# Optimization experiments

Hardware: AMD Instinct MI355X
Metric: run time of the kernel (lower is better)

The kernel has to match this reference:

```python
import jax, jax.numpy as jnp
import numpy as np

N = 4096      # num nodes
E = 131072    # num edges
D = 128       # embed dim (in=out)
HID = 16      # kan hidden dim
G, K = 4, 3   # KAN grid_size / spline_order (GCN + FFN kans)
GA, KA = 2, 1 # attention KANLinear grid_size / spline_order
H, HD = 8, 16 # heads, head_dim

def make_grid(in_f, g, k):
    h = 2.0 / g
    pts = (np.arange(-k, g + k + 1) * h - 1.0).astype(np.float32)  # [g+2k+1]
    return jnp.asarray(np.tile(pts[None, :], (in_f, 1)))            # [in_f, g+2k+1]

GRID_D = make_grid(D, G, K)
GRID_H = make_grid(HID, G, K)
GRID_A = make_grid(D, GA, KA)

def b_splines(x, grid, k):
    # x: [n, in] -> B-spline bases [n, in, g+k] via Cox-de-Boor recursion
    x = x[:, :, None]
    g = grid[None]
    bases = ((x >= g[..., :-1]) & (x < g[..., 1:])).astype(x.dtype)
    for j in range(1, k + 1):
        bases = ((x - g[..., :-(j + 1)]) / (g[..., j:-1] - g[..., :-(j + 1)]) * bases[..., :-1]
                 + (g[..., j + 1:] - x) / (g[..., j + 1:] - g[..., 1:-j]) * bases[..., 1:])
    return bases

def kan_lin(x, bw, sw, grid, k, use_silu):
    base = jax.nn.silu(x) if use_silu else x
    return base @ bw.T + jnp.einsum('nig,oig->no', b_splines(x, grid, k), sw)

def ekan2(x, bw1, sw1, bw2, sw2):
    # eKAN with layers_hidden=[D, HID, D], SiLU base activation
    h = kan_lin(x, bw1, sw1, GRID_D, K, True)
    return kan_lin(h, bw2, sw2, GRID_H, K, True)

def layer_norm(h, s, b):
    m = jnp.mean(h, axis=-1, keepdims=True)
    v = jnp.var(h, axis=-1, keepdims=True)
    return (h - m) * jax.lax.rsqrt(v + 1e-5) * s + b

def setup_inputs() -> dict:
    key = jax.random.key(0)
    ks = jax.random.split(key, 20)
    r = lambda i, shape: jax.random.normal(ks[i], shape, jnp.float32) * 0.1
    return dict(
        x=jax.random.normal(ks[0], (N, D), jnp.float32),
        edge_index=jax.random.randint(ks[1], (2, E), 0, N),
        gcn_bw1=r(2, (HID, D)), gcn_sw1=r(3, (HID, D, G + K)),
        gcn_bw2=r(4, (D, HID)), gcn_sw2=r(5, (D, HID, G + K)),
        q_bw=r(6, (D, D)), q_sw=r(7, (D, D, GA + KA)),
        k_bw=r(8, (D, D)), k_sw=r(9, (D, D, GA + KA)),
        v_bw=r(10, (D, D)), v_sw=r(11, (D, D, GA + KA)),
        ffn_bw1=r(12, (HID, D)), ffn_sw1=r(13, (HID, D, G + K)),
        ffn_bw2=r(14, (D, HID)), ffn_sw2=r(15, (D, HID, G + K)),
        ln1_s=jnp.ones(D), ln1_b=jnp.zeros(D),
        ln2_s=jnp.ones(D), ln2_b=jnp.zeros(D),
        ln3_s=jnp.ones(D), ln3_b=jnp.zeros(D),
    )

def reference(x, edge_index, gcn_bw1, gcn_sw1, gcn_bw2, gcn_sw2,
              q_bw, q_sw, k_bw, k_sw, v_bw, v_sw,
              ffn_bw1, ffn_sw1, ffn_bw2, ffn_sw2,
              ln1_s, ln1_b, ln2_s, ln2_b, ln3_s, ln3_b):
    n = x.shape[0]
    # ---- local GCN-KAN branch: KAN(A_hat x) ----
    loops = jnp.arange(n)
    row = jnp.concatenate([edge_index[0], loops])  # sources (+ self-loops)
    col = jnp.concatenate([edge_index[1], loops])  # targets
    w = jnp.ones(row.shape[0], x.dtype)
    deg = jax.ops.segment_sum(w, row, num_segments=n)
    dis = jnp.where(deg > 0, deg ** -0.5, 0.0)
    norm = dis[row] * w * dis[col]
    agg = jax.ops.segment_sum(norm[:, None] * x[row], col, num_segments=n)  # [n, D]
    h_local = ekan2(agg, gcn_bw1, gcn_sw1, gcn_bw2, gcn_sw2)
    h_local = layer_norm(x + h_local, ln1_s, ln1_b)
    # ---- global KAN multi-head attention branch ----
    Q = kan_lin(x, q_bw, q_sw, GRID_A, KA, False).reshape(n, H, HD)
    Kv = kan_lin(x, k_bw, k_sw, GRID_A, KA, False).reshape(n, H, HD)
    V = kan_lin(x, v_bw, v_sw, GRID_A, KA, False).reshape(n, H, HD)
    scores = jnp.einsum('nhd,mhd->hnm', Q, Kv) / np.sqrt(HD)  # [H, n, n]
    attn = jax.nn.softmax(scores, axis=-1)
    h_attn = jnp.einsum('hnm,mhd->nhd', attn, V).reshape(n, D)
    h_attn = layer_norm(x + h_attn, ln2_s, ln2_b)
    # ---- combine + KAN feed-forward ----
    h = h_local + h_attn
    out = layer_norm(h + ekan2(h, ffn_bw1, ffn_sw1, ffn_bw2, ffn_sw2), ln3_s, ln3_b)
    return out
```

## Files before the change

### kernel.cpp

```cpp
#include <hip/hip_runtime.h>

typedef unsigned short u16;
typedef unsigned int u32;

#define D_ 128
#define HID_ 16
#define NH_ 8
#define HD_ 16
#define PSTRIDE 17

#define WE_W1G 0
#define WE_W2G 16384
#define WE_W1F 32768
#define WE_W2F 49152
#define WE_TOTAL 65536

#define KROW 24
#define VROW 136
#define PROW 40
#define HROW 136

typedef __attribute__((ext_vector_type(8))) short bfrag;
typedef __attribute__((ext_vector_type(4))) float ffrag;


__device__ __forceinline__ float bf2f(u16 u) {
    union { u32 i; float f; } v; v.i = ((u32)u) << 16; return v.f;
}
__device__ __forceinline__ u16 f2bf(float f) {
    u32 x = __float_as_uint(f);
    u32 r = (x + 0x7fffu + ((x >> 16) & 1u)) >> 16;
    return (u16)r;
}
__device__ __forceinline__ float rdf(const void* p, int i, bool bf) {
    return bf ? bf2f(((const u16*)p)[i]) : ((const float*)p)[i];
}

__device__ __forceinline__ u32 probe_stat(const u16* p) {
    for (int i = 0; i < 128; i++) {
        u16 u = p[i];
        int e = (u >> 7) & 0xFF;
        int m = u & 0x7F;
        bool zero = (e == 0) && (m == 0);
        bool sane = zero || (e >= 97 && e <= 147);
        if (!sane) return 0u;
    }
    return 1u;
}

__global__ void k_detect(const void* x,
                         const void* gbw1, const void* gsw1, const void* gbw2, const void* gsw2,
                         const void* qbw, const void* qsw, const void* kbw, const void* ksw,
                         const void* vbw, const void* vsw,
                         const void* fbw1, const void* fsw1, const void* fbw2, const void* fsw2,
                         const void* l1s, const void* l1b, const void* l2s, const void* l2b,
                         const void* l3s, const void* l3b,
                         u32* flags) {
    int t = threadIdx.x;
    const void* ptrs[21] = {x, gbw1, gsw1, gbw2, gsw2, qbw, qsw, kbw, ksw, vbw, vsw,
                            fbw1, fsw1, fbw2, fsw2, l1s, l1b, l2s, l2b, l3s, l3b};
    if (t < 21) {
        u32 f = 0;
        if (t == 15 || t == 17 || t == 19) {
            f = (((const u32*)ptrs[t])[0] != 0x3F800000u) ? 1u : 0u;
        } else if (t == 16 || t == 18 || t == 20) {
            f = 0;
        } else {
            f = probe_stat((const u16*)ptrs[t]);
        }
        flags[t] = f;
    }
    __syncthreads();
    if (t == 16 || t == 18 || t == 20) flags[t] = flags[t - 1];
}

__device__ __forceinline__ float cub_seg(float s) {
    if (s < 0.0f || s >= 4.0f) return 0.0f;
    if (s < 1.0f) return s * s * s * (1.0f / 6.0f);
    if (s < 2.0f) { float r = s - 1.0f; return (1.0f + 3.0f * r + 3.0f * r * r - 3.0f * r * r * r) * (1.0f / 6.0f); }
    if (s < 3.0f) { float r = s - 2.0f; return (4.0f - 6.0f * r * r + 3.0f * r * r * r) * (1.0f / 6.0f); }
    float q = 4.0f - s; return q * q * q * (1.0f / 6.0f);
}
__device__ __forceinline__ float lin_seg(float s) {
    if (s < 0.0f || s >= 2.0f) return 0.0f;
    return (s < 1.0f) ? s : (2.0f - s);
}

__device__ __forceinline__ float bsum(float v, float* tmp) {
#pragma unroll
    for (int off = 1; off < 64; off <<= 1) v += __shfl_xor(v, off, 64);
    __syncthreads();
    if ((threadIdx.x & 63) == 0) tmp[threadIdx.x >> 6] = v;
    __syncthreads();
    return tmp[0] + tmp[1];
}

__device__ __forceinline__ uint4 feat8(float a) {
    float si = a / (1.0f + __expf(-a));
    float u = (a + 2.5f) * 2.0f;
    float b0 = cub_seg(u), b1 = cub_seg(u - 1.0f), b2 = cub_seg(u - 2.0f), b3 = cub_seg(u - 3.0f);
    float b4 = cub_seg(u - 4.0f), b5 = cub_seg(u - 5.0f), b6 = cub_seg(u - 6.0f);
    uint4 r;
    r.x = (u32)f2bf(si) | ((u32)f2bf(b0) << 16);
    r.y = (u32)f2bf(b1) | ((u32)f2bf(b2) << 16);
    r.z = (u32)f2bf(b3) | ((u32)f2bf(b4) << 16);
    r.w = (u32)f2bf(b5) | ((u32)f2bf(b6) << 16);
    return r;
}

__global__ void k_conv4(const void* __restrict__ x,
                        const void* l1s, const void* l1b, const void* l2s,
                        const void* l2b, const void* l3s, const void* l3b,
                        const u32* __restrict__ flags,
                        float* __restrict__ xin, float* __restrict__ lnp,
                        u16* __restrict__ F,
                        int* __restrict__ cnt, int* __restrict__ fill,
                        int* __restrict__ degi, int N) {
    int total = N * D_ + 768 + 3 * N;
    bool bfx = flags[0] != 0;
    for (int i = blockIdx.x * 256 + threadIdx.x; i < total; i += gridDim.x * 256) {
        if (i < N * D_) {
            float xv = rdf(x, i, bfx);
            xin[i] = xv;
            float u = xv + 2.0f;
            u32 lo = (u32)f2bf(xv) | ((u32)f2bf(lin_seg(u)) << 16);
            u32 hi = (u32)f2bf(lin_seg(u - 1.0f)) | ((u32)f2bf(lin_seg(u - 2.0f)) << 16);
            ((uint2*)F)[i] = make_uint2(lo, hi);
        } else {
            int j = i - N * D_;
            if (j < 768) {
                int sel = j >> 7, k = j & 127;
                const void* p = sel == 0 ? l1s : sel == 1 ? l1b : sel == 2 ? l2s
                             : sel == 3 ? l2b : sel == 4 ? l3s : l3b;
                lnp[j] = rdf(p, k, flags[15 + sel] != 0);
            } else {
                int j2 = j - 768;
                if (j2 < N) cnt[j2] = 0;
                else if (j2 < 2 * N) fill[j2 - N] = 0;
                else degi[j2 - 2 * N] = 0;
            }
        }
    }
}

__global__ void k_pack(const void* gbw1, const void* gsw1, const void* gbw2, const void* gsw2,
                       const void* fbw1, const void* fsw1, const void* fbw2, const void* fsw2,
                       const void* qbw, const void* qsw, const void* kbw, const void* ksw,
                       const void* vbw, const void* vsw,
                       const u32* __restrict__ flags,
                       u16* __restrict__ Web, u16* __restrict__ Wb) {
    int t = blockIdx.x * 256 + threadIdx.x;
    if (t < 8192) {
        int seg = t >> 11, i = t & 2047;
        const void* bw = seg == 0 ? gbw1 : seg == 1 ? gbw2 : seg == 2 ? fbw1 : fbw2;
        const void* sw = seg == 0 ? gsw1 : seg == 1 ? gsw2 : seg == 2 ? fsw1 : fsw2;
        int fb = seg == 0 ? 1 : seg == 1 ? 3 : seg == 2 ? 11 : 13;
        bool bwbf = flags[fb] != 0, swbf = flags[fb + 1] != 0;
        u16* dst = Web + (size_t)seg * 16384 + (size_t)i * 8;
        dst[0] = f2bf(rdf(bw, i, bwbf));
#pragma unroll
        for (int g = 0; g < 7; g++) dst[1 + g] = f2bf(rdf(sw, i * 7 + g, swbf));
    } else if (t < 8192 + 49152) {
        int uu = t - 8192;
        int seg = uu >> 14, i = uu & 16383;
        const void* bw = seg == 0 ? qbw : seg == 1 ? kbw : vbw;
        const void* sw = seg == 0 ? qsw : seg == 1 ? ksw : vsw;
        int fb = 5 + seg * 2;
        bool bwbf = flags[fb] != 0, swbf = flags[fb + 1] != 0;
        float sc = (seg == 0) ? 0.25f : 1.0f;
        u16* dst = Wb + (size_t)seg * 65536 + (size_t)i * 4;
        dst[0] = f2bf(rdf(bw, i, bwbf) * sc);
#pragma unroll
        for (int g = 0; g < 3; g++) dst[1 + g] = f2bf(rdf(sw, i * 3 + g, swbf) * sc);
    }
}

__global__ void k_count(const int* __restrict__ ei, int* __restrict__ cnt,
                        int* __restrict__ degi, int E) {
    int e = blockIdx.x * 256 + threadIdx.x;
    if (e < E) {
        atomicAdd(&degi[ei[e]], 1);
        atomicAdd(&cnt[ei[E + e]], 1);
    }
}
__global__ __launch_bounds__(1024) void k_scan(const int* __restrict__ cnt,
                                               const int* __restrict__ degi,
                                               int* __restrict__ rowptr,
                                               float* __restrict__ dis, int N) {
    __shared__ int s[1024];
    int t = threadIdx.x;
    int base = t * 4;
    int a[4];
#pragma unroll
    for (int k = 0; k < 4; k++) a[k] = (base + k < N) ? cnt[base + k] : 0;
    int loc = a[0] + a[1] + a[2] + a[3];
    s[t] = loc;
    __syncthreads();
    for (int off = 1; off < 1024; off <<= 1) {
        int v = (t >= off) ? s[t - off] : 0;
        __syncthreads();
        s[t] += v;
        __syncthreads();
    }
    int ex = s[t] - loc;
    int run = ex;
#pragma unroll
    for (int k = 0; k < 4; k++) {
        if (base + k < N) rowptr[base + k] = run;
        run += a[k];
    }
    if (t == 1023) rowptr[N] = s[1023];
#pragma unroll
    for (int k = 0; k < 4; k++)
        if (base + k < N) dis[base + k] = rsqrtf((float)degi[base + k] + 1.0f);
}
__global__ void k_fill(const int* __restrict__ ei, const int* __restrict__ rowptr,
                       int* __restrict__ fill, int* __restrict__ elist, int E) {
    int e = blockIdx.x * 256 + threadIdx.x;
    if (e < E) {
        int r = ei[e], c = ei[E + e];
        int pos = rowptr[c] + atomicAdd(&fill[c], 1);
        elist[pos] = r;
    }
}

__global__ __launch_bounds__(128) void k_gcn(const int* __restrict__ rowptr,
        const int* __restrict__ elist, const float* __restrict__ dis,
        const float* __restrict__ xin, u16* __restrict__ Afeat) {
    int c = blockIdx.x, t = threadIdx.x;
    __shared__ int ids[128];
    __shared__ float wsh[128];
    int beg = rowptr[c], end = rowptr[c + 1];
    float acc = 0.0f;
    for (int j0 = beg; j0 < end; j0 += 128) {
        int cc = min(128, end - j0);
        __syncthreads();
        if (t < cc) {
            int rr = elist[j0 + t];
            ids[t] = rr;
            wsh[t] = dis[rr];
        }
        __syncthreads();
        for (int j = 0; j < cc; j++)
            acc += wsh[j] * xin[(size_t)ids[j] * D_ + t];
    }
    float dc = dis[c];
    float a = dc * (acc + dc * xin[(size_t)c * D_ + t]);
    ((uint4*)Afeat)[(size_t)c * D_ + t] = feat8(a);
}

__global__ __launch_bounds__(64) void k_ekan_mm(const u16* __restrict__ A,
        const u16* __restrict__ W1b, const u16* __restrict__ W2b,
        const float* __restrict__ resid,
        const float* __restrict__ lns, const float* __restrict__ lnb,
        void* __restrict__ outp, const u32* __restrict__ flags, int fin, int N) {
    __shared__ u16 hfL[16 * HROW];
    int mt = blockIdx.x;
    int lane = threadIdx.x, quad = lane >> 4, l15 = lane & 15;
    const u16* ar = A + (size_t)(mt * 16 + l15) * 1024 + quad * 8;
    const u16* br = W1b + (size_t)l15 * 1024 + quad * 8;
    ffrag acc = {0, 0, 0, 0};
#pragma unroll
    for (int ks = 0; ks < 1024; ks += 32) {
        bfrag af = *(const bfrag*)(ar + ks);
        bfrag bf = *(const bfrag*)(br + ks);
        acc = __builtin_amdgcn_mfma_f32_16x16x32_bf16(af, bf, acc, 0, 0, 0);
    }
#define G1EPI(RR, COMP) { \
    uint4 fv = feat8(acc.COMP); \
    *(uint4*)(&hfL[(quad * 4 + RR) * HROW + l15 * 8]) = fv; }
    G1EPI(0, x) G1EPI(1, y) G1EPI(2, z) G1EPI(3, w)
#undef G1EPI
    __asm__ volatile("s_waitcnt lgkmcnt(0)" ::: "memory");
    __builtin_amdgcn_wave_barrier();
    const u16* b0 = W2b + (size_t)l15 * 128 + quad * 8;
    ffrag a0 = {0,0,0,0}, a1 = {0,0,0,0}, a2 = {0,0,0,0}, a3 = {0,0,0,0};
    ffrag a4 = {0,0,0,0}, a5 = {0,0,0,0}, a6 = {0,0,0,0}, a7 = {0,0,0,0};
#pragma unroll
    for (int ks = 0; ks < 128; ks += 32) {
        bfrag af = *(const bfrag*)(&hfL[l15 * HROW + quad * 8 + ks]);
        a0 = __builtin_amdgcn_mfma_f32_16x16x32_bf16(af, *(const bfrag*)(b0 + 0 * 2048 + ks), a0, 0, 0, 0);
        a1 = __builtin_amdgcn_mfma_f32_16x16x32_bf16(af, *(const bfrag*)(b0 + 1 * 2048 + ks), a1, 0, 0, 0);
        a2 = __builtin_amdgcn_mfma_f32_16x16x32_bf16(af, *(const bfrag*)(b0 + 2 * 2048 + ks), a2, 0, 0, 0);
        a3 = __builtin_amdgcn_mfma_f32_16x16x32_bf16(af, *(const bfrag*)(b0 + 3 * 2048 + ks), a3, 0, 0, 0);
        a4 = __builtin_amdgcn_mfma_f32_16x16x32_bf16(af, *(const bfrag*)(b0 + 4 * 2048 + ks), a4, 0, 0, 0);
        a5 = __builtin_amdgcn_mfma_f32_16x16x32_bf16(af, *(const bfrag*)(b0 + 5 * 2048 + ks), a5, 0, 0, 0);
        a6 = __builtin_amdgcn_mfma_f32_16x16x32_bf16(af, *(const bfrag*)(b0 + 6 * 2048 + ks), a6, 0, 0, 0);
        a7 = __builtin_amdgcn_mfma_f32_16x16x32_bf16(af, *(const bfrag*)(b0 + 7 * 2048 + ks), a7, 0, 0, 0);
    }
    float ls0 = lns[l15],       lb0 = lnb[l15];
    float ls1 = lns[16 + l15],  lb1 = lnb[16 + l15];
    float ls2 = lns[32 + l15],  lb2 = lnb[32 + l15];
    float ls3 = lns[48 + l15],  lb3 = lnb[48 + l15];
    float ls4 = lns[64 + l15],  lb4 = lnb[64 + l15];
    float ls5 = lns[80 + l15],  lb5 = lnb[80 + l15];
    float ls6 = lns[96 + l15],  lb6 = lnb[96 + l15];
    float ls7 = lns[112 + l15], lb7 = lnb[112 + l15];
    bool bfo = (fin != 0) && (flags[0] != 0);
#define G2EPI(RR, COMP) { \
    int node = mt * 16 + quad * 4 + RR; \
    const float* rr_ = resid + (size_t)node * 128 + l15; \
    float v0 = a0.COMP + rr_[0];   float v1 = a1.COMP + rr_[16]; \
    float v2 = a2.COMP + rr_[32];  float v3 = a3.COMP + rr_[48]; \
    float v4 = a4.COMP + rr_[64];  float v5 = a5.COMP + rr_[80]; \
    float v6 = a6.COMP + rr_[96];  float v7 = a7.COMP + rr_[112]; \
    float s1 = ((v0 + v1) + (v2 + v3)) + ((v4 + v5) + (v6 + v7)); \
    float s2 = ((v0*v0 + v1*v1) + (v2*v2 + v3*v3)) + ((v4*v4 + v5*v5) + (v6*v6 + v7*v7)); \
    s1 += __shfl_xor(s1, 1, 64); s2 += __shfl_xor(s2, 1, 64); \
    s1 += __shfl_xor(s1, 2, 64); s2 += __shfl_xor(s2, 2, 64); \
    s1 += __shfl_xor(s1, 4, 64); s2 += __shfl_xor(s2, 4, 64); \
    s1 += __shfl_xor(s1, 8, 64); s2 += __shfl_xor(s2, 8, 64); \
    float mean = s1 * 0.0078125f; \
    float var = s2 * 0.0078125f - mean * mean; \
    float rs = rsqrtf(var + 1e-5f); \
    float y0 = (v0 - mean) * rs * ls0 + lb0; float y1 = (v1 - mean) * rs * ls1 + lb1; \
    float y2 = (v2 - mean) * rs * ls2 + lb2; float y3 = (v3 - mean) * rs * ls3 + lb3; \
    float y4 = (v4 - mean) * rs * ls4 + lb4; float y5 = (v5 - mean) * rs * ls5 + lb5; \
    float y6 = (v6 - mean) * rs * ls6 + lb6; float y7 = (v7 - mean) * rs * ls7 + lb7; \
    if (bfo) { \
        u16* ob = (u16*)outp + (size_t)node * 128 + l15; \
        ob[0] = f2bf(y0); ob[16] = f2bf(y1); ob[32] = f2bf(y2); ob[48] = f2bf(y3); \
        ob[64] = f2bf(y4); ob[80] = f2bf(y5); ob[96] = f2bf(y6); ob[112] = f2bf(y7); \
    } else { \
        float* ob = (float*)outp + (size_t)node * 128 + l15; \
        ob[0] = y0; ob[16] = y1; ob[32] = y2; ob[48] = y3; \
        ob[64] = y4; ob[80] = y5; ob[96] = y6; ob[112] = y7; \
    } }
    G2EPI(0, x) G2EPI(1, y) G2EPI(2, z) G2EPI(3, w)
#undef G2EPI
}

#define QKV_STORE(ACC, TL) { \
    int col = cg * 48 + (TL) * 16 + l15; \
    int mat = col >> 7, idx = col & 127; \
    u16* dstb = (mat == 0) ? Qb : (mat == 1) ? Kb : Vb; \
    size_t base = (size_t)(idx >> 4) * N * HD_ + (size_t)(idx & 15); \
    dstb[base + (size_t)(rowb + 0) * HD_] = f2bf(ACC.x); \
    dstb[base + (size_t)(rowb + 1) * HD_] = f2bf(ACC.y); \
    dstb[base + (size_t)(rowb + 2) * HD_] = f2bf(ACC.z); \
    dstb[base + (size_t)(rowb + 3) * HD_] = f2bf(ACC.w); \
}

__global__ __launch_bounds__(64) void k_qkv5(const u16* __restrict__ F,
        const u16* __restrict__ Wb,
        u16* __restrict__ Qb, u16* __restrict__ Kb, u16* __restrict__ Vb, int N) {
    int mt = blockIdx.x, cg = blockIdx.y;
    int lane = threadIdx.x, quad = lane >> 4, l15 = lane & 15;
    const u16* arow = F + (size_t)(mt * 16 + l15) * 512 + quad * 8;
    const u16* b0r = Wb + (size_t)(cg * 48 + l15) * 512 + quad * 8;
    const u16* b1r = b0r + 16 * 512;
    const u16* b2r = b0r + 32 * 512;
    ffrag a0 = {0, 0, 0, 0}, a1 = {0, 0, 0, 0}, a2 = {0, 0, 0, 0};
#pragma unroll
    for (int ks = 0; ks < 512; ks += 32) {
        bfrag af = *(const bfrag*)(arow + ks);
        bfrag bf0 = *(const bfrag*)(b0r + ks);
        bfrag bf1 = *(const bfrag*)(b1r + ks);
        bfrag bf2 = *(const bfrag*)(b2r + ks);
        a0 = __builtin_amdgcn_mfma_f32_16x16x32_bf16(af, bf0, a0, 0, 0, 0);
        a1 = __builtin_amdgcn_mfma_f32_16x16x32_bf16(af, bf1, a1, 0, 0, 0);
        a2 = __builtin_amdgcn_mfma_f32_16x16x32_bf16(af, bf2, a2, 0, 0, 0);
    }
    int rowb = mt * 16 + quad * 4;
    QKV_STORE(a0, 0)
    QKV_STORE(a1, 1)
    QKV_STORE(a2, 2)
}

#define ATTN_SCORE(QF, LACC, PBT) { \
    ffrag zz = {0.0f, 0.0f, 0.0f, 0.0f}; \
    ffrag s0 = __builtin_amdgcn_mfma_f32_16x16x32_bf16(QF, kf0, zz, 0, 0, 0); \
    ffrag s1 = __builtin_amdgcn_mfma_f32_16x16x32_bf16(QF, kf1, zz, 0, 0, 0); \
    float a0 = __expf(s0.x), a1 = __expf(s0.y), a2 = __expf(s0.z), a3 = __expf(s0.w); \
    float b0 = __expf(s1.x), b1 = __expf(s1.y), b2 = __expf(s1.z), b3 = __expf(s1.w); \
    LACC.x += a0 + b0; LACC.y += a1 + b1; LACC.z += a2 + b2; LACC.w += a3 + b3; \
    u32* pw = (u32*)PBT; \
    pw[(quad * 4 + 0) * (PROW / 2) + l15] = (__float_as_uint(a0) >> 16) | (__float_as_uint(b0) & 0xFFFF0000u); \
    pw[(quad * 4 + 1) * (PROW / 2) + l15] = (__float_as_uint(a1) >> 16) | (__float_as_uint(b1) & 0xFFFF0000u); \
    pw[(quad * 4 + 2) * (PROW / 2) + l15] = (__float_as_uint(a2) >> 16) | (__float_as_uint(b2) & 0xFFFF0000u); \
    pw[(quad * 4 + 3) * (PROW / 2) + l15] = (__float_as_uint(a3) >> 16) | (__float_as_uint(b3) & 0xFFFF0000u); \
}

#define ATTN_PV(OACC, PBT) { \
    bfrag pf = *(const bfrag*)(&PBT[l15 * PROW + quad * 8]); \
    OACC = __builtin_amdgcn_mfma_f32_16x16x32_bf16(pf, vf, OACC, 0, 0, 0); \
}

#define STORE_TILE(OACC, LACC, TL) { \
    int q0 = qtb + (TL) * 16 + quad * 4; \
    float* pp; \
    pp = part + ((size_t)(h * N + q0 + 0) * SPLIT + s) * PSTRIDE; \
    pp[1 + l15] = OACC.x; if (l15 == 0) pp[0] = LACC.x; \
    pp = part + ((size_t)(h * N + q0 + 1) * SPLIT + s) * PSTRIDE; \
    pp[1 + l15] = OACC.y; if (l15 == 0) pp[0] = LACC.y; \
    pp = part + ((size_t)(h * N + q0 + 2) * SPLIT + s) * PSTRIDE; \
    pp[1 + l15] = OACC.z; if (l15 == 0) pp[0] = LACC.z; \
    pp = part + ((size_t)(h * N + q0 + 3) * SPLIT + s) * PSTRIDE; \
    pp[1 + l15] = OACC.w; if (l15 == 0) pp[0] = LACC.w; \
}

__global__ __launch_bounds__(256) void k_attn9(const u16* __restrict__ Qb,
        const u16* __restrict__ Kb, const u16* __restrict__ Vb,
        float* __restrict__ part, int N, int SPLIT) {
    int s = blockIdx.x, qb = blockIdx.y, h = blockIdx.z;
    int t = threadIdx.x;
    int w = t >> 6, lane = t & 63, quad = lane >> 4, l15 = lane & 15;
    __shared__ u16 ldsK[128 * KROW + 16];
    __shared__ u16 ldsVt[16 * VROW];
    __shared__ u16 ldsP[4][4][16 * PROW];

    const u16* qrow = Qb + (size_t)h * N * HD_;
    const u16* krow = Kb + (size_t)h * N * HD_;
    const u16* vrow = Vb + (size_t)h * N * HD_;

    for (int i = t; i < (128 * KROW + 16) / 2; i += 256) ((u32*)ldsK)[i] = 0;

    int qtb = qb * 256 + w * 64;
    bfrag qz = {0, 0, 0, 0, 0, 0, 0, 0};
    bfrag qf0 = qz, qf1 = qz, qf2 = qz, qf3 = qz;
    if (quad < 2) {
        qf0 = *(const bfrag*)(qrow + (size_t)(qtb + 0 * 16 + l15) * HD_ + quad * 8);
        qf1 = *(const bfrag*)(qrow + (size_t)(qtb + 1 * 16 + l15) * HD_ + quad * 8);
        qf2 = *(const bfrag*)(qrow + (size_t)(qtb + 2 * 16 + l15) * HD_ + quad * 8);
        qf3 = *(const bfrag*)(qrow + (size_t)(qtb + 3 * 16 + l15) * HD_ + quad * 8);
    }

    ffrag o0 = {0, 0, 0, 0}, o1 = {0, 0, 0, 0}, o2 = {0, 0, 0, 0}, o3 = {0, 0, 0, 0};
    ffrag L0 = {0, 0, 0, 0}, L1 = {0, 0, 0, 0}, L2 = {0, 0, 0, 0}, L3 = {0, 0, 0, 0};
    u16* pb0 = &ldsP[w][0][0];
    u16* pb1 = &ldsP[w][1][0];
    u16* pb2 = &ldsP[w][2][0];
    u16* pb3 = &ldsP[w][3][0];

    int keys = N / SPLIT;
    int kstart0 = s * keys;
    for (int kst = 0; kst < keys; kst += 128) {
        int kg = kstart0 + kst;
        __syncthreads();
        if (t < 128) {
            const uint4* src = (const uint4*)(krow + (size_t)(kg + t) * HD_);
            uint4 a = src[0], b = src[1];
            *(uint4*)(&ldsK[t * KROW]) = a;
            *(uint4*)(&ldsK[t * KROW + 8]) = b;
        } else {
            int key = t - 128;
            const uint4* src = (const uint4*)(vrow + (size_t)(kg + key) * HD_);
            uint4 a = src[0], b = src[1];
            ldsVt[0 * VROW + key] = (u16)(a.x);  ldsVt[1 * VROW + key] = (u16)(a.x >> 16);
            ldsVt[2 * VROW + key] = (u16)(a.y);  ldsVt[3 * VROW + key] = (u16)(a.y >> 16);
            ldsVt[4 * VROW + key] = (u16)(a.z);  ldsVt[5 * VROW + key] = (u16)(a.z >> 16);
            ldsVt[6 * VROW + key] = (u16)(a.w);  ldsVt[7 * VROW + key] = (u16)(a.w >> 16);
            ldsVt[8 * VROW + key] = (u16)(b.x);  ldsVt[9 * VROW + key] = (u16)(b.x >> 16);
            ldsVt[10 * VROW + key] = (u16)(b.y); ldsVt[11 * VROW + key] = (u16)(b.y >> 16);
            ldsVt[12 * VROW + key] = (u16)(b.z); ldsVt[13 * VROW + key] = (u16)(b.z >> 16);
            ldsVt[14 * VROW + key] = (u16)(b.w); ldsVt[15 * VROW + key] = (u16)(b.w >> 16);
        }
        __syncthreads();
#pragma unroll
        for (int koff = 0; koff < 128; koff += 32) {
            bfrag kf0 = *(const bfrag*)(&ldsK[(koff + 2 * l15) * KROW + quad * 8]);
            bfrag kf1 = *(const bfrag*)(&ldsK[(koff + 2 * l15 + 1) * KROW + quad * 8]);
            bfrag vf = *(const bfrag*)(&ldsVt[l15 * VROW + koff + quad * 8]);
            ATTN_SCORE(qf0, L0, pb0)
            ATTN_SCORE(qf1, L1, pb1)
            ATTN_SCORE(qf2, L2, pb2)
            ATTN_SCORE(qf3, L3, pb3)
            __asm__ volatile("s_waitcnt lgkmcnt(0)" ::: "memory");
            ATTN_PV(o0, pb0)
            ATTN_PV(o1, pb1)
            ATTN_PV(o2, pb2)
            ATTN_PV(o3, pb3)
        }
    }

#pragma unroll
    for (int off = 1; off < 16; off <<= 1) {
        L0.x += __shfl_xor(L0.x, off, 64); L0.y += __shfl_xor(L0.y, off, 64);
        L0.z += __shfl_xor(L0.z, off, 64); L0.w += __shfl_xor(L0.w, off, 64);
        L1.x += __shfl_xor(L1.x, off, 64); L1.y += __shfl_xor(L1.y, off, 64);
        L1.z += __shfl_xor(L1.z, off, 64); L1.w += __shfl_xor(L1.w, off, 64);
        L2.x += __shfl_xor(L2.x, off, 64); L2.y += __shfl_xor(L2.y, off, 64);
        L2.z += __shfl_xor(L2.z, off, 64); L2.w += __shfl_xor(L2.w, off, 64);
        L3.x += __shfl_xor(L3.x, off, 64); L3.y += __shfl_xor(L3.y, off, 64);
        L3.z += __shfl_xor(L3.z, off, 64); L3.w += __shfl_xor(L3.w, off, 64);
    }
    STORE_TILE(o0, L0, 0)
    STORE_TILE(o1, L1, 1)
    STORE_TILE(o2, L2, 2)
    STORE_TILE(o3, L3, 3)
}

__global__ __launch_bounds__(128) void k_comb(const float* __restrict__ part,
        const float* __restrict__ xin, const float* __restrict__ hl,
        const float* __restrict__ lnp, float* __restrict__ hv,
        u16* __restrict__ Afeat, int N, int SPLIT) {
    int n = blockIdx.x, t = threadIdx.x;
    __shared__ float red[128];
    int h = t >> 4, d = t & 15;
    float L = 0.0f, O = 0.0f;
    for (int ss = 0; ss < SPLIT; ss++) {
        const float* ps = part + ((size_t)(h * N + n) * SPLIT + ss) * PSTRIDE;
        L += ps[0];
        O += ps[1 + d];
    }
    float ha = O / L;
    float r = xin[(size_t)n * D_ + t] + ha;
    float mean = bsum(r, red) * (1.0f / 128.0f);
    float c = r - mean;
    float var = bsum(c * c, red) * (1.0f / 128.0f);
    float y2 = c * rsqrtf(var + 1e-5f) * lnp[256 + t] + lnp[384 + t];
    float hvv = hl[(size_t)n * D_ + t] + y2;
    hv[(size_t)n * D_ + t] = hvv;
    ((uint4*)Afeat)[(size_t)n * D_ + t] = feat8(hvv);
}

extern "C" void kernel_launch(void* const* d_in, const int* in_sizes, int n_in,
                              void* d_out, int out_size, void* d_ws, size_t ws_size,
                              hipStream_t stream) {
    const void* x = d_in[0];
    const int* ei = (const int*)d_in[1];
    const void* gbw1 = d_in[2];
    const void* gsw1 = d_in[3];
    const void* gbw2 = d_in[4];
    const void* gsw2 = d_in[5];
    const void* qbw = d_in[6];
    const void* qsw = d_in[7];
    const void* kbw = d_in[8];
    const void* ksw = d_in[9];
    const void* vbw = d_in[10];
    const void* vsw = d_in[11];
    const void* fbw1 = d_in[12];
    const void* fsw1 = d_in[13];
    const void* fbw2 = d_in[14];
    const void* fsw2 = d_in[15];
    const void* ln1s = d_in[16];
    const void* ln1b = d_in[17];
    const void* ln2s = d_in[18];
    const void* ln2b = d_in[19];
    const void* ln3s = d_in[20];
    const void* ln3b = d_in[21];

    const int N = in_sizes[0] / D_;
    const int E = in_sizes[1] / 2;
    const size_t ND = (size_t)N * D_;

    float* wf = (float*)d_ws;
    u32* flags = (u32*)wf;
    float* lnp = wf + 32;
    float* dis = wf + 800;
    float* xin = dis + N;
    float* hl  = xin + ND;
    float* hv  = hl + ND;
    u16* Web = (u16*)(hv + ND);
    u16* Wb  = Web + WE_TOTAL;
    u16* F   = Wb + 196608;
    u16* Qb  = F + (size_t)N * 512;
    u16* Kb  = Qb + ND;
    u16* Vb  = Kb + ND;
    u16* Afeat = Vb + ND;
    int* cnt    = (int*)(Afeat + (size_t)N * 1024);
    int* fill   = cnt + N;
    int* degi   = fill + N;
    int* rowptr = degi + N;
    int* elist  = rowptr + N + 1;
    float* part = (float*)(elist + E);

    size_t baseBytes = (size_t)((char*)part - (char*)d_ws);
    int SPLIT = 16;
    if (baseBytes + (size_t)NH_ * N * 16 * PSTRIDE * 4 > ws_size) SPLIT = 8;
    if (baseBytes + (size_t)NH_ * N * 8 * PSTRIDE * 4 > ws_size) SPLIT = 4;

    k_detect<<<1, 64, 0, stream>>>(x, gbw1, gsw1, gbw2, gsw2, qbw, qsw, kbw, ksw,
                                   vbw, vsw, fbw1, fsw1, fbw2, fsw2,
                                   ln1s, ln1b, ln2s, ln2b, ln3s, ln3b, flags);
    k_conv4<<<1024, 256, 0, stream>>>(x, ln1s, ln1b, ln2s, ln2b, ln3s, ln3b,
                                      flags, xin, lnp, F, cnt, fill, degi, N);
    k_pack<<<224, 256, 0, stream>>>(gbw1, gsw1, gbw2, gsw2, fbw1, fsw1, fbw2, fsw2,
                                    qbw, qsw, kbw, ksw, vbw, vsw, flags, Web, Wb);
    k_count<<<(E + 255) / 256, 256, 0, stream>>>(ei, cnt, degi, E);
    k_scan<<<1, 1024, 0, stream>>>(cnt, degi, rowptr, dis, N);
    k_fill<<<(E + 255) / 256, 256, 0, stream>>>(ei, rowptr, fill, elist, E);
    k_gcn<<<N, 128, 0, stream>>>(rowptr, elist, dis, xin, Afeat);
    k_ekan_mm<<<N / 16, 64, 0, stream>>>(Afeat, Web + WE_W1G, Web + WE_W2G, xin,
                                         lnp + 0, lnp + 128, hl, flags, 0, N);
    k_qkv5<<<dim3(N / 16, 8), 64, 0, stream>>>(F, Wb, Qb, Kb, Vb, N);
    k_attn9<<<dim3(SPLIT, N / 256, NH_), 256, 0, stream>>>(Qb, Kb, Vb, part, N, SPLIT);
    k_comb<<<N, 128, 0, stream>>>(part, xin, hl, lnp, hv, Afeat, N, SPLIT);
    k_ekan_mm<<<N / 16, 64, 0, stream>>>(Afeat, Web + WE_W1F, Web + WE_W2F, hv,
                                         lnp + 512, lnp + 640, d_out, flags, 1, N);
}
```

Before: 244.2 us.

## Merge setup kernels, warp-shuffle scan, exp2 softmax, halve attention split

Folds the conversion, weight packing and edge counting kernels into one launch and moves the counter zeroing into the detect kernel, cutting launch count and serialization. It also rewrites the single-block prefix scan to use wavefront shuffles instead of a barrier-heavy shared-memory loop. The GCN gather loop gets two accumulators, and attention uses exp2 with log2(e) folded into the Q scale. The default attention split drops from 16 to 8, which changes parallelism against partial-combine work. Zeroing 3N ints from a single 256-thread block adds serial work at the start.

```diff
diff --git a/kernel.cpp b/kernel.cpp
--- a/kernel.cpp
+++ b/kernel.cpp
@@ -20,8 +20,19 @@
 #define PROW 40
 #define HROW 136
 
+#define QSCALE 0.3606737602222409f
+
 typedef __attribute__((ext_vector_type(8))) short bfrag;
 typedef __attribute__((ext_vector_type(4))) float ffrag;
+
+#if defined(__has_builtin)
+#if __has_builtin(__builtin_amdgcn_exp2f)
+#define EXP2F(x) __builtin_amdgcn_exp2f(x)
+#endif
+#endif
+#ifndef EXP2F
+#define EXP2F(x) exp2f(x)
+#endif
 
 
 __device__ __forceinline__ float bf2f(u16 u) {
@@ -48,14 +59,14 @@
     return 1u;
 }
 
-__global__ void k_detect(const void* x,
+__global__ __launch_bounds__(256) void k_detect(const void* x,
                          const void* gbw1, const void* gsw1, const void* gbw2, const void* gsw2,
                          const void* qbw, const void* qsw, const void* kbw, const void* ksw,
                          const void* vbw, const void* vsw,
                          const void* fbw1, const void* fsw1, const void* fbw2, const void* fsw2,
                          const void* l1s, const void* l1b, const void* l2s, const void* l2b,
                          const void* l3s, const void* l3b,
-                         u32* flags) {
+                         u32* flags, int* __restrict__ cnt3, int N) {
     int t = threadIdx.x;
     const void* ptrs[21] = {x, gbw1, gsw1, gbw2, gsw2, qbw, qsw, kbw, ksw, vbw, vsw,
                             fbw1, fsw1, fbw2, fsw2, l1s, l1b, l2s, l2b, l3s, l3b};
@@ -72,6 +83,8 @@
     }
     __syncthreads();
     if (t == 16 || t == 18 || t == 20) flags[t] = flags[t - 1];
+    int tot = 3 * N;
+    for (int i = t; i < tot; i += 256) cnt3[i] = 0;
 }
 
 __device__ __forceinline__ float cub_seg(float s) {
@@ -108,112 +121,114 @@
     return r;
 }
 
-__global__ void k_conv4(const void* __restrict__ x,
-                        const void* l1s, const void* l1b, const void* l2s,
-                        const void* l2b, const void* l3s, const void* l3b,
-                        const u32* __restrict__ flags,
-                        float* __restrict__ xin, float* __restrict__ lnp,
-                        u16* __restrict__ F,
-                        int* __restrict__ cnt, int* __restrict__ fill,
-                        int* __restrict__ degi, int N) {
-    int total = N * D_ + 768 + 3 * N;
-    bool bfx = flags[0] != 0;
-    for (int i = blockIdx.x * 256 + threadIdx.x; i < total; i += gridDim.x * 256) {
+__global__ __launch_bounds__(256) void k_setup(const void* __restrict__ x,
+        const void* l1s, const void* l1b, const void* l2s,
+        const void* l2b, const void* l3s, const void* l3b,
+        const void* gbw1, const void* gsw1, const void* gbw2, const void* gsw2,
+        const void* fbw1, const void* fsw1, const void* fbw2, const void* fsw2,
+        const void* qbw, const void* qsw, const void* kbw, const void* ksw,
+        const void* vbw, const void* vsw,
+        const int* __restrict__ ei,
+        const u32* __restrict__ flags,
+        float* __restrict__ xin, float* __restrict__ lnp,
+        u16* __restrict__ F,
+        u16* __restrict__ Web, u16* __restrict__ Wb,
+        int* __restrict__ cnt, int* __restrict__ degi,
+        int N, int E) {
+    int b = blockIdx.x;
+    int convB = ((N * D_ + 768) + 255) >> 8;
+    if (b < convB) {
+        int i = b * 256 + threadIdx.x;
         if (i < N * D_) {
-            float xv = rdf(x, i, bfx);
+            float xv = rdf(x, i, flags[0] != 0);
             xin[i] = xv;
             float u = xv + 2.0f;
             u32 lo = (u32)f2bf(xv) | ((u32)f2bf(lin_seg(u)) << 16);
             u32 hi = (u32)f2bf(lin_seg(u - 1.0f)) | ((u32)f2bf(lin_seg(u - 2.0f)) << 16);
             ((uint2*)F)[i] = make_uint2(lo, hi);
-        } else {
+        } else if (i < N * D_ + 768) {
             int j = i - N * D_;
-            if (j < 768) {
-                int sel = j >> 7, k = j & 127;
-                const void* p = sel == 0 ? l1s : sel == 1 ? l1b : sel == 2 ? l2s
-                             : sel == 3 ? l2b : sel == 4 ? l3s : l3b;
-                lnp[j] = rdf(p, k, flags[15 + sel] != 0);
-            } else {
-                int j2 = j - 768;
-                if (j2 < N) cnt[j2] = 0;
-                else if (j2 < 2 * N) fill[j2 - N] = 0;
-                else degi[j2 - 2 * N] = 0;
-            }
-        }
-    }
-}
-
-__global__ void k_pack(const void* gbw1, const void* gsw1, const void* gbw2, const void* gsw2,
-                       const void* fbw1, const void* fsw1, const void* fbw2, const void* fsw2,
-                       const void* qbw, const void* qsw, const void* kbw, const void* ksw,
-                       const void* vbw, const void* vsw,
-                       const u32* __restrict__ flags,
-                       u16* __restrict__ Web, u16* __restrict__ Wb) {
-    int t = blockIdx.x * 256 + threadIdx.x;
-    if (t < 8192) {
-        int seg = t >> 11, i = t & 2047;
-        const void* bw = seg == 0 ? gbw1 : seg == 1 ? gbw2 : seg == 2 ? fbw1 : fbw2;
-        const void* sw = seg == 0 ? gsw1 : seg == 1 ? gsw2 : seg == 2 ? fsw1 : fsw2;
-        int fb = seg == 0 ? 1 : seg == 1 ? 3 : seg == 2 ? 11 : 13;
-        bool bwbf = flags[fb] != 0, swbf = flags[fb + 1] != 0;
-        u16* dst = Web + (size_t)seg * 16384 + (size_t)i * 8;
-        dst[0] = f2bf(rdf(bw, i, bwbf));
-#pragma unroll
-        for (int g = 0; g < 7; g++) dst[1 + g] = f2bf(rdf(sw, i * 7 + g, swbf));
-    } else if (t < 8192 + 49152) {
-        int uu = t - 8192;
-        int seg = uu >> 14, i = uu & 16383;
-        const void* bw = seg == 0 ? qbw : seg == 1 ? kbw : vbw;
-        const void* sw = seg == 0 ? qsw : seg == 1 ? ksw : vsw;
-        int fb = 5 + seg * 2;
-        bool bwbf = flags[fb] != 0, swbf = flags[fb + 1] != 0;
-        float sc = (seg == 0) ? 0.25f : 1.0f;
-        u16* dst = Wb + (size_t)seg * 65536 + (size_t)i * 4;
-        dst[0] = f2bf(rdf(bw, i, bwbf) * sc);
-#pragma unroll
-        for (int g = 0; g < 3; g++) dst[1 + g] = f2bf(rdf(sw, i * 3 + g, swbf) * sc);
-    }
-}
-
-__global__ void k_count(const int* __restrict__ ei, int* __restrict__ cnt,
-                        int* __restrict__ degi, int E) {
-    int e = blockIdx.x * 256 + threadIdx.x;
-    if (e < E) {
-        atomicAdd(&degi[ei[e]], 1);
-        atomicAdd(&cnt[ei[E + e]], 1);
-    }
-}
+            int sel = j >> 7, k = j & 127;
+            const void* p = sel == 0 ? l1s : sel == 1 ? l1b : sel == 2 ? l2s
+                         : sel == 3 ? l2b : sel == 4 ? l3s : l3b;
+            lnp[j] = rdf(p, k, flags[15 + sel] != 0);
+        }
+    } else if (b < convB + 224) {
+        int t = (b - convB) * 256 + threadIdx.x;
+        if (t < 8192) {
+            int seg = t >> 11, i = t & 2047;
+            const void* bw = seg == 0 ? gbw1 : seg == 1 ? gbw2 : seg == 2 ? fbw1 : fbw2;
+            const void* sw = seg == 0 ? gsw1 : seg == 1 ? gsw2 : seg == 2 ? fsw1 : fsw2;
+            int fb = seg == 0 ? 1 : seg == 1 ? 3 : seg == 2 ? 11 : 13;
+            bool bwbf = flags[fb] != 0, swbf = flags[fb + 1] != 0;
+            u16* dst = Web + (size_t)seg * 16384 + (size_t)i * 8;
+            dst[0] = f2bf(rdf(bw, i, bwbf));
+#pragma unroll
+            for (int g = 0; g < 7; g++) dst[1 + g] = f2bf(rdf(sw, i * 7 + g, swbf));
+        } else if (t < 8192 + 49152) {
+            int uu = t - 8192;
+            int seg = uu >> 14, i = uu & 16383;
+            const void* bw = seg == 0 ? qbw : seg == 1 ? kbw : vbw;
+            const void* sw = seg == 0 ? qsw : seg == 1 ? ksw : vsw;
+            int fb = 5 + seg * 2;
+            bool bwbf = flags[fb] != 0, swbf = flags[fb + 1] != 0;
+            float sc = (seg == 0) ? QSCALE : 1.0f;
+            u16* dst = Wb + (size_t)seg * 65536 + (size_t)i * 4;
+            dst[0] = f2bf(rdf(bw, i, bwbf) * sc);
+#pragma unroll
+            for (int g = 0; g < 3; g++) dst[1 + g] = f2bf(rdf(sw, i * 3 + g, swbf) * sc);
+        }
+    } else {
+        int e = (b - convB - 224) * 256 + threadIdx.x;
+        if (e < E) {
+            atomicAdd(&degi[ei[e]], 1);
+            atomicAdd(&cnt[ei[E + e]], 1);
+        }
+    }
+}
+
 __global__ __launch_bounds__(1024) void k_scan(const int* __restrict__ cnt,
                                                const int* __restrict__ degi,
                                                int* __restrict__ rowptr,
                                                float* __restrict__ dis, int N) {
-    __shared__ int s[1024];
+    __shared__ int ws[16];
     int t = threadIdx.x;
     int base = t * 4;
     int a[4];
 #pragma unroll
     for (int k = 0; k < 4; k++) a[k] = (base + k < N) ? cnt[base + k] : 0;
     int loc = a[0] + a[1] + a[2] + a[3];
-    s[t] = loc;
+    int pre = loc;
+#pragma unroll
+    for (int off = 1; off < 64; off <<= 1) {
+        int v = __shfl_up(pre, off, 64);
+        if ((t & 63) >= off) pre += v;
+    }
+    if ((t & 63) == 63) ws[t >> 6] = pre;
     __syncthreads();
-    for (int off = 1; off < 1024; off <<= 1) {
-        int v = (t >= off) ? s[t - off] : 0;
-        __syncthreads();
-        s[t] += v;
-        __syncthreads();
-    }
-    int ex = s[t] - loc;
+    if (t < 64) {
+        int v = (t < 16) ? ws[t] : 0;
+#pragma unroll
+        for (int off = 1; off < 16; off <<= 1) {
+            int u = __shfl_up(v, off, 64);
+            if (t >= off) v += u;
+        }
+        if (t < 16) ws[t] = v;
+    }
+    __syncthreads();
+    int ex = pre - loc + ((t >= 64) ? ws[(t >> 6) - 1] : 0);
     int run = ex;
 #pragma unroll
     for (int k = 0; k < 4; k++) {
         if (base + k < N) rowptr[base + k] = run;
         run += a[k];
     }
-    if (t == 1023) rowptr[N] = s[1023];
+    if (t == 1023) rowptr[N] = ws[15];
 #pragma unroll
     for (int k = 0; k < 4; k++)
         if (base + k < N) dis[base + k] = rsqrtf((float)degi[base + k] + 1.0f);
 }
+
 __global__ void k_fill(const int* __restrict__ ei, const int* __restrict__ rowptr,
                        int* __restrict__ fill, int* __restrict__ elist, int E) {
     int e = blockIdx.x * 256 + threadIdx.x;
@@ -231,7 +246,7 @@
     __shared__ int ids[128];
     __shared__ float wsh[128];
     int beg = rowptr[c], end = rowptr[c + 1];
-    float acc = 0.0f;
+    float acc = 0.0f, acc2 = 0.0f;
     for (int j0 = beg; j0 < end; j0 += 128) {
         int cc = min(128, end - j0);
         __syncthreads();
@@ -241,11 +256,15 @@
             wsh[t] = dis[rr];
         }
         __syncthreads();
-        for (int j = 0; j < cc; j++)
-            acc += wsh[j] * xin[(size_t)ids[j] * D_ + t];
+        int j = 0;
+        for (; j + 2 <= cc; j += 2) {
+            acc  += wsh[j]     * xin[(size_t)ids[j] * D_ + t];
+            acc2 += wsh[j + 1] * xin[(size_t)ids[j + 1] * D_ + t];
+        }
+        if (j < cc) acc += wsh[j] * xin[(size_t)ids[j] * D_ + t];
     }
     float dc = dis[c];
-    float a = dc * (acc + dc * xin[(size_t)c * D_ + t]);
+    float a = dc * (acc + acc2 + dc * xin[(size_t)c * D_ + t]);
     ((uint4*)Afeat)[(size_t)c * D_ + t] = feat8(a);
 }
 
@@ -371,8 +390,8 @@
     ffrag zz = {0.0f, 0.0f, 0.0f, 0.0f}; \
     ffrag s0 = __builtin_amdgcn_mfma_f32_16x16x32_bf16(QF, kf0, zz, 0, 0, 0); \
     ffrag s1 = __builtin_amdgcn_mfma_f32_16x16x32_bf16(QF, kf1, zz, 0, 0, 0); \
-    float a0 = __expf(s0.x), a1 = __expf(s0.y), a2 = __expf(s0.z), a3 = __expf(s0.w); \
-    float b0 = __expf(s1.x), b1 = __expf(s1.y), b2 = __expf(s1.z), b3 = __expf(s1.w); \
+    float a0 = EXP2F(s0.x), a1 = EXP2F(s0.y), a2 = EXP2F(s0.z), a3 = EXP2F(s0.w); \
+    float b0 = EXP2F(s1.x), b1 = EXP2F(s1.y), b2 = EXP2F(s1.z), b3 = EXP2F(s1.w); \
     LACC.x += a0 + b0; LACC.y += a1 + b1; LACC.z += a2 + b2; LACC.w += a3 + b3; \
     u32* pw = (u32*)PBT; \
     pw[(quad * 4 + 0) * (PROW / 2) + l15] = (__float_as_uint(a0) >> 16) | (__float_as_uint(b0) & 0xFFFF0000u); \
@@ -566,20 +585,23 @@
     float* part = (float*)(elist + E);
 
     size_t baseBytes = (size_t)((char*)part - (char*)d_ws);
-    int SPLIT = 16;
-    if (baseBytes + (size_t)NH_ * N * 16 * PSTRIDE * 4 > ws_size) SPLIT = 8;
+    int SPLIT = 8;
     if (baseBytes + (size_t)NH_ * N * 8 * PSTRIDE * 4 > ws_size) SPLIT = 4;
-
-    k_detect<<<1, 64, 0, stream>>>(x, gbw1, gsw1, gbw2, gsw2, qbw, qsw, kbw, ksw,
-                                   vbw, vsw, fbw1, fsw1, fbw2, fsw2,
-                                   ln1s, ln1b, ln2s, ln2b, ln3s, ln3b, flags);
-    k_conv4<<<1024, 256, 0, stream>>>(x, ln1s, ln1b, ln2s, ln2b, ln3s, ln3b,
-                                      flags, xin, lnp, F, cnt, fill, degi, N);
-    k_pack<<<224, 256, 0, stream>>>(gbw1, gsw1, gbw2, gsw2, fbw1, fsw1, fbw2, fsw2,
-                                    qbw, qsw, kbw, ksw, vbw, vsw, flags, Web, Wb);
-    k_count<<<(E + 255) / 256, 256, 0, stream>>>(ei, cnt, degi, E);
+    if (baseBytes + (size_t)NH_ * N * 4 * PSTRIDE * 4 > ws_size) SPLIT = 2;
+
+    int convB = ((N * D_ + 768) + 255) >> 8;
+    int countB = (E + 255) / 256;
+
+    k_detect<<<1, 256, 0, stream>>>(x, gbw1, gsw1, gbw2, gsw2, qbw, qsw, kbw, ksw,
+                                    vbw, vsw, fbw1, fsw1, fbw2, fsw2,
+                                    ln1s, ln1b, ln2s, ln2b, ln3s, ln3b, flags, cnt, N);
+    k_setup<<<convB + 224 + countB, 256, 0, stream>>>(
+        x, ln1s, ln1b, ln2s, ln2b, ln3s, ln3b,
+        gbw1, gsw1, gbw2, gsw2, fbw1, fsw1, fbw2, fsw2,
+        qbw, qsw, kbw, ksw, vbw, vsw,
+        ei, flags, xin, lnp, F, Web, Wb, cnt, degi, N, E);
     k_scan<<<1, 1024, 0, stream>>>(cnt, degi, rowptr, dis, N);
-    k_fill<<<(E + 255) / 256, 256, 0, stream>>>(ei, rowptr, fill, elist, E);
+    k_fill<<<countB, 256, 0, stream>>>(ei, rowptr, fill, elist, E);
     k_gcn<<<N, 128, 0, stream>>>(rowptr, elist, dis, xin, Afeat);
     k_ekan_mm<<<N / 16, 64, 0, stream>>>(Afeat, Web + WE_W1G, Web + WE_W2G, xin,
                                          lnp + 0, lnp + 128, hl, flags, 0, N);
```

Result: no change. 241.7 us (-1.0%).
